# Optimization experiments

Hardware: AMD Instinct MI355X
Metric: run time of the kernel (lower is better)

Reference implementation:

```python
import jax, jax.numpy as jnp
import numpy as np
from jax import lax

IMG_H, IMG_W = 800, 800           # self.image_size
GRID = 64                         # feature map H=W
STRIDE = IMG_H // GRID            # torchvision AnchorGenerator stride
ANCHOR_SIZE = 32.0                # sizes=(32,), aspect_ratios=(1.0,)
PRE_NMS_TOP_N = 500
POST_NMS_TOP_N = 500
NMS_THRESH = 0.7
MIN_BOX_SIZE = 0.001
MIN_BOX_SCORE = 0.0


def make_anchors(h, w, stride):
    # torchvision single-size, ratio-1 base anchor centered at origin: [-16,-16,16,16]
    half = ANCHOR_SIZE / 2.0
    base = jnp.array([-half, -half, half, half], dtype=jnp.float32)
    sx = jnp.arange(w, dtype=jnp.float32) * stride
    sy = jnp.arange(h, dtype=jnp.float32) * stride
    yy, xx = jnp.meshgrid(sy, sx, indexing='ij')
    shifts = jnp.stack([xx, yy, xx, yy], axis=-1).reshape(-1, 4)  # [HW,4], row-major over (y,x)
    return shifts + base  # [HW,4] in (x1,y1,x2,y2)


def decode_boxes(reg, anchors):
    # reg: [B,N,4] (dx,dy,dw,dh); anchors: [N,4]
    wa = anchors[:, 2] - anchors[:, 0]
    ha = anchors[:, 3] - anchors[:, 1]
    cxa = anchors[:, 0] + 0.5 * wa
    cya = anchors[:, 1] + 0.5 * ha
    dx, dy, dw, dh = reg[..., 0], reg[..., 1], reg[..., 2], reg[..., 3]
    cx = dx * wa + cxa
    cy = dy * ha + cya
    w = jnp.exp(dw) * wa
    h = jnp.exp(dh) * ha
    return jnp.stack([cx - 0.5 * w, cy - 0.5 * h, cx + 0.5 * w, cy + 0.5 * h], axis=-1)


def clip_boxes(boxes):
    x = jnp.clip(boxes[..., 0::2], 0.0, float(IMG_W))
    y = jnp.clip(boxes[..., 1::2], 0.0, float(IMG_H))
    out = jnp.stack([x[..., 0], y[..., 0], x[..., 1], y[..., 1]], axis=-1)
    return out


def pairwise_iou(boxes):
    # boxes: [N,4] -> iou [N,N]
    area = (boxes[:, 2] - boxes[:, 0]) * (boxes[:, 3] - boxes[:, 1])
    lt = jnp.maximum(boxes[:, None, :2], boxes[None, :, :2])
    rb = jnp.minimum(boxes[:, None, 2:], boxes[None, :, 2:])
    wh = jnp.clip(rb - lt, 0.0)
    inter = wh[..., 0] * wh[..., 1]
    return inter / (area[:, None] + area[None, :] - inter + 1e-9)


def nms_keep(boxes, valid):
    # boxes already sorted by descending score (topk output). Greedy NMS.
    n = boxes.shape[0]
    iou = pairwise_iou(boxes)
    idx = jnp.arange(n)

    def body(i, keep):
        suppress = keep[i] & (iou[i] > NMS_THRESH) & (idx > i)
        return keep & jnp.logical_not(suppress)

    return lax.fori_loop(0, n, body, valid)


def setup_inputs() -> dict:
    key = jax.random.key(0)
    ks = jax.random.split(key, 4)
    B, C, H, W = 4, 512, GRID, GRID
    feature_map = jax.random.normal(ks[0], (B, C, H, W), dtype=jnp.float32)
    conv_w = jax.random.normal(ks[1], (512, 512, 3, 3), dtype=jnp.float32) * 0.02
    conv_b = jnp.zeros((512,), dtype=jnp.float32)
    score_w = jax.random.normal(ks[2], (1, 512), dtype=jnp.float32) * 0.01
    score_b = jnp.zeros((1,), dtype=jnp.float32)
    bbox_w = jax.random.normal(ks[3], (4, 512), dtype=jnp.float32) * 0.01
    bbox_b = jnp.zeros((4,), dtype=jnp.float32)
    return {"feature_map": feature_map, "conv_w": conv_w, "conv_b": conv_b,
            "score_w": score_w, "score_b": score_b, "bbox_w": bbox_w, "bbox_b": bbox_b}


def reference(feature_map, conv_w, conv_b, score_w, score_b, bbox_w, bbox_b):
    B, C, H, W = feature_map.shape
    # common_feature_extractor: 3x3 conv + ReLU
    f = lax.conv_general_dilated(feature_map, conv_w, (1, 1), 'SAME',
                                 dimension_numbers=('NCHW', 'OIHW', 'NCHW'))
    f = jax.nn.relu(f + conv_b[None, :, None, None])
    # 1x1 heads
    object_score = jnp.einsum('bchw,oc->bohw', f, score_w) + score_b[None, :, None, None]  # [B,1,H,W]
    bbox_reg = jnp.einsum('bchw,oc->bohw', f, bbox_w) + bbox_b[None, :, None, None]        # [B,4,H,W]
    # reshape (B,4,-1).permute(0,2,1) -> [B,N,4]
    reg = jnp.transpose(bbox_reg.reshape(B, 4, -1), (0, 2, 1))
    anchors = make_anchors(H, W, STRIDE)                 # [N,4]
    proposals = decode_boxes(reg, anchors)               # [B,N,4]
    logits = object_score.reshape(B, -1)                 # [B,N]
    # filter_proposals: topk on detached logits
    top_vals, top_idx = lax.top_k(lax.stop_gradient(logits), PRE_NMS_TOP_N)  # sorted desc
    props = jnp.take_along_axis(proposals, top_idx[..., None], axis=1)       # [B,500,4]
    probs = jax.nn.sigmoid(top_vals)                                          # [B,500]
    props = clip_boxes(props)
    ws = props[..., 2] - props[..., 0]
    hs = props[..., 3] - props[..., 1]
    valid = (ws >= MIN_BOX_SIZE) & (hs >= MIN_BOX_SIZE) & (probs >= MIN_BOX_SCORE)
    keep = jax.vmap(nms_keep)(props, valid)               # [B,500] (post_nms_top_n == pre, no truncation)
    final_props = props * keep[..., None].astype(props.dtype)
    final_scores = probs * keep.astype(probs.dtype)
    return f, final_props, final_scores, keep
```

## Files before the change

### kernel.cpp

```cpp
#include <hip/hip_runtime.h>
#include <math.h>

#define BB   4
#define CC   512
#define HH   64
#define WW   64
#define NN   4096
#define TOPK 500

typedef _Float16 half8 __attribute__((ext_vector_type(8)));
typedef float f32x16   __attribute__((ext_vector_type(16)));

__device__ __forceinline__ void split_f16(float v, _Float16& h, _Float16& l) {
    h = (_Float16)v;
    l = (_Float16)(v - (float)h);
}

__global__ __launch_bounds__(256) void prepack_w_kernel(
    const float* __restrict__ w, _Float16* __restrict__ wh,
    _Float16* __restrict__ wl)
{
    const int t = blockIdx.x * 256 + threadIdx.x;
    if (t >= 512 * 32) return;
    const int co = t & 511;
    const int cb = t >> 9;
    const float* src = w + (size_t)co * 4608 + cb * 144;
#pragma unroll
    for (int tap = 0; tap < 9; ++tap) {
        half8 h0, h1, l0, l1;
#pragma unroll
        for (int i = 0; i < 8; ++i) {
            _Float16 h, l;
            split_f16(src[i * 9 + tap] * 4096.0f, h, l);
            h0[i] = h; l0[i] = l;
            split_f16(src[(i + 8) * 9 + tap] * 4096.0f, h, l);
            h1[i] = h; l1[i] = l;
        }
        const size_t dst = ((size_t)(tap * 32 + cb) * 512 + co) * 16;
        *(half8*)(wh + dst)     = h0;
        *(half8*)(wh + dst + 8) = h1;
        *(half8*)(wl + dst)     = l0;
        *(half8*)(wl + dst + 8) = l1;
    }
}

__global__ __launch_bounds__(256) void conv3x3_mfma_kernel(
    const float* __restrict__ x, const _Float16* __restrict__ wh,
    const _Float16* __restrict__ wl, const float* __restrict__ bias,
    float* __restrict__ out)
{
    __shared__ __align__(16) _Float16 xs_h[4][66][24];
    __shared__ __align__(16) _Float16 xs_l[4][66][24];

    const int tid  = threadIdx.x;
    const int lane = tid & 63;
    const int wave = tid >> 6;
    const int wco  = wave & 1;
    const int wpx  = wave >> 1;
    const int kg   = lane >> 5;
    const int ln   = lane & 31;

    const int co_blk = blockIdx.x * 128;
    const int r0     = blockIdx.y * 2;
    const int b      = blockIdx.z;

    const float* xb = x + (size_t)b * CC * NN;

    const int s_ci   = tid & 15;
    const int s_sub  = tid >> 4;
    const int s_row  = s_sub & 3;
    const int s_colg = s_sub >> 2;

    f32x16 acc[2][2];
#pragma unroll
    for (int mt = 0; mt < 2; ++mt)
#pragma unroll
        for (int nt = 0; nt < 2; ++nt)
#pragma unroll
            for (int r = 0; r < 16; ++r) acc[mt][nt][r] = 0.f;

    half8 Ah[2][2], Al[2][2];

    for (int cb = 0; cb < 32; ++cb) {
        const int gr = r0 - 1 + s_row;
        float vals[16];
        if ((unsigned)gr < 64u) {
            const float* p = xb + (size_t)(cb * 16 + s_ci) * NN + gr * 64 + s_colg * 16;
            *(float4*)&vals[0]  = *(const float4*)(p + 0);
            *(float4*)&vals[4]  = *(const float4*)(p + 4);
            *(float4*)&vals[8]  = *(const float4*)(p + 8);
            *(float4*)&vals[12] = *(const float4*)(p + 12);
        } else {
#pragma unroll
            for (int j = 0; j < 16; ++j) vals[j] = 0.f;
        }
        __syncthreads();
#pragma unroll
        for (int j = 0; j < 16; ++j) {
            _Float16 h, l;
            split_f16(vals[j] * 4096.0f, h, l);
            const int c = 1 + s_colg * 16 + j;
            xs_h[s_row][c][s_ci] = h;
            xs_l[s_row][c][s_ci] = l;
        }
        if (tid < 128) {
            const int ci = tid & 15, rr = (tid >> 4) & 3, side = (tid >> 6) & 1;
            xs_h[rr][side * 65][ci] = (_Float16)0.f;
            xs_l[rr][side * 65][ci] = (_Float16)0.f;
        }
        __syncthreads();

        {
            const size_t base = (size_t)(0 * 32 + cb) * 512;
#pragma unroll
            for (int mt = 0; mt < 2; ++mt) {
                const int co_w = co_blk + wco * 64 + mt * 32 + ln;
                const size_t o = (base + co_w) * 16 + kg * 8;
                Ah[0][mt] = *(const half8*)(wh + o);
                Al[0][mt] = *(const half8*)(wl + o);
            }
        }
#pragma unroll
        for (int tap = 0; tap < 9; ++tap) {
            const int pb = tap & 1, pn = pb ^ 1;
            if (tap < 8) {
                const size_t base = (size_t)((tap + 1) * 32 + cb) * 512;
#pragma unroll
                for (int mt = 0; mt < 2; ++mt) {
                    const int co_w = co_blk + wco * 64 + mt * 32 + ln;
                    const size_t o = (base + co_w) * 16 + kg * 8;
                    Ah[pn][mt] = *(const half8*)(wh + o);
                    Al[pn][mt] = *(const half8*)(wl + o);
                }
            }
            const int dy = tap / 3, dx = tap % 3;
            half8 Bh[2], Bl[2];
#pragma unroll
            for (int nt = 0; nt < 2; ++nt) {
                const int c = nt * 32 + ln + dx;
                Bh[nt] = *(const half8*)&xs_h[wpx + dy][c][kg * 8];
                Bl[nt] = *(const half8*)&xs_l[wpx + dy][c][kg * 8];
            }
#pragma unroll
            for (int mt = 0; mt < 2; ++mt)
#pragma unroll
                for (int nt = 0; nt < 2; ++nt) {
                    acc[mt][nt] = __builtin_amdgcn_mfma_f32_32x32x16_f16(
                        Al[pb][mt], Bh[nt], acc[mt][nt], 0, 0, 0);
                    acc[mt][nt] = __builtin_amdgcn_mfma_f32_32x32x16_f16(
                        Ah[pb][mt], Bl[nt], acc[mt][nt], 0, 0, 0);
                    acc[mt][nt] = __builtin_amdgcn_mfma_f32_32x32x16_f16(
                        Ah[pb][mt], Bh[nt], acc[mt][nt], 0, 0, 0);
                }
        }
    }

    const float inv_scale = 5.9604644775390625e-08f;
    const int himg = r0 + wpx;
#pragma unroll
    for (int mt = 0; mt < 2; ++mt)
#pragma unroll
        for (int nt = 0; nt < 2; ++nt) {
            const int wimg = nt * 32 + ln;
#pragma unroll
            for (int reg = 0; reg < 16; ++reg) {
                const int co = co_blk + wco * 64 + mt * 32 +
                               (reg & 3) + 8 * (reg >> 2) + 4 * kg;
                float v = fmaf(acc[mt][nt][reg], inv_scale, bias[co]);
                v = v > 0.f ? v : 0.f;
                out[(((size_t)b * CC + co) * HH + himg) * WW + wimg] = v;
            }
        }
}

__global__ __launch_bounds__(256) void conv3x3_relu_kernel(
    const float* __restrict__ x, const float* __restrict__ wgt,
    const float* __restrict__ bias, float* __restrict__ out)
{
    __shared__ float xs[8][6][66];
    __shared__ float wsh[8][9][64];
    const int co_base = blockIdx.x * 64;
    const int r0 = blockIdx.y * 4;
    const int b  = blockIdx.z;
    const int tid = threadIdx.x;
    const int col = tid & 63;
    const int co_off = (tid >> 6) * 16;

    float acc[4][16];
#pragma unroll
    for (int r = 0; r < 4; ++r)
#pragma unroll
        for (int k = 0; k < 16; ++k) acc[r][k] = 0.f;

    const float* xb = x + (size_t)b * CC * HH * WW;

    for (int cb = 0; cb < CC; cb += 8) {
        __syncthreads();
        for (int idx = tid; idx < 8 * 6 * 66; idx += 256) {
            int cc = idx % 66;
            int rest = idx / 66;
            int rr = rest % 6;
            int ci = rest / 6;
            int gr = r0 - 1 + rr;
            int gc = cc - 1;
            float v = 0.f;
            if (gr >= 0 && gr < HH && (unsigned)gc < (unsigned)WW)
                v = xb[((cb + ci) * HH + gr) * WW + gc];
            xs[ci][rr][cc] = v;
        }
        for (int idx = tid; idx < 8 * 9 * 64; idx += 256) {
            int co = idx & 63;
            int rest = idx >> 6;
            int ci = rest / 9;
            int tap = rest - ci * 9;
            wsh[ci][tap][co] = wgt[(size_t)(co_base + co) * (CC * 9) + (cb + ci) * 9 + tap];
        }
        __syncthreads();
#pragma unroll
        for (int ci = 0; ci < 8; ++ci) {
#pragma unroll
            for (int kh = 0; kh < 3; ++kh) {
                float xv[4][3];
#pragma unroll
                for (int r = 0; r < 4; ++r)
#pragma unroll
                    for (int kw = 0; kw < 3; ++kw)
                        xv[r][kw] = xs[ci][r + kh][col + kw];
#pragma unroll
                for (int kw = 0; kw < 3; ++kw) {
#pragma unroll
                    for (int k = 0; k < 16; k += 4) {
                        float4 wv = *(const float4*)&wsh[ci][kh * 3 + kw][co_off + k];
#pragma unroll
                        for (int r = 0; r < 4; ++r) {
                            acc[r][k + 0] = fmaf(xv[r][kw], wv.x, acc[r][k + 0]);
                            acc[r][k + 1] = fmaf(xv[r][kw], wv.y, acc[r][k + 1]);
                            acc[r][k + 2] = fmaf(xv[r][kw], wv.z, acc[r][k + 2]);
                            acc[r][k + 3] = fmaf(xv[r][kw], wv.w, acc[r][k + 3]);
                        }
                    }
                }
            }
        }
    }
#pragma unroll
    for (int k = 0; k < 16; ++k) {
        const int co = co_base + co_off + k;
        const float bv = bias[co];
#pragma unroll
        for (int r = 0; r < 4; ++r) {
            float v = acc[r][k] + bv;
            v = v > 0.f ? v : 0.f;
            out[(((size_t)b * CC + co) * HH + (r0 + r)) * WW + col] = v;
        }
    }
}

__global__ __launch_bounds__(256) void heads_decode_kernel(
    const float* __restrict__ f, const float* __restrict__ score_w,
    const float* __restrict__ score_b, const float* __restrict__ bbox_w,
    const float* __restrict__ bbox_b,
    float* __restrict__ logits, float* __restrict__ props)
{
    __shared__ float sw[CC];
    __shared__ float bw0[CC], bw1[CC], bw2[CC], bw3[CC];
    const int tid = threadIdx.x;
    for (int i = tid; i < CC; i += 256) {
        sw[i]  = score_w[i];
        bw0[i] = bbox_w[0 * CC + i];
        bw1[i] = bbox_w[1 * CC + i];
        bw2[i] = bbox_w[2 * CC + i];
        bw3[i] = bbox_w[3 * CC + i];
    }
    __syncthreads();
    const int b = blockIdx.y;
    const int n = blockIdx.x * 256 + tid;
    const float* fb = f + (size_t)b * CC * NN + n;
    float s = 0.f, d0 = 0.f, d1 = 0.f, d2 = 0.f, d3 = 0.f;
    for (int ci = 0; ci < CC; ++ci) {
        float v = fb[(size_t)ci * NN];
        s  = fmaf(v, sw[ci],  s);
        d0 = fmaf(v, bw0[ci], d0);
        d1 = fmaf(v, bw1[ci], d1);
        d2 = fmaf(v, bw2[ci], d2);
        d3 = fmaf(v, bw3[ci], d3);
    }
    s  += score_b[0];
    d0 += bbox_b[0]; d1 += bbox_b[1]; d2 += bbox_b[2]; d3 += bbox_b[3];
    logits[b * NN + n] = s;
    const int hx = n & 63, hy = n >> 6;
    const float cxa = 12.f * (float)hx, cya = 12.f * (float)hy;
    const float cx = d0 * 32.f + cxa;
    const float cy = d1 * 32.f + cya;
    const float w2 = expf(d2) * 16.f;
    const float h2 = expf(d3) * 16.f;
    float* p = props + ((size_t)b * NN + n) * 4;
    p[0] = cx - w2; p[1] = cy - h2; p[2] = cx + w2; p[3] = cy + h2;
}

__global__ __launch_bounds__(1024) void topk_kernel(
    const float* __restrict__ logits, const float* __restrict__ props,
    float* __restrict__ props500, float* __restrict__ probs500,
    unsigned long long* __restrict__ validb)
{
    __shared__ float sv[NN];
    __shared__ int   si[NN];
    const int b = blockIdx.x;
    const int tid = threadIdx.x;
    for (int i = tid; i < NN; i += 1024) { sv[i] = logits[b * NN + i]; si[i] = i; }
    __syncthreads();
    for (int k = 2; k <= NN; k <<= 1) {
        for (int j = k >> 1; j > 0; j >>= 1) {
            for (int t = tid; t < NN / 2; t += 1024) {
                const int i = ((t & ~(j - 1)) << 1) | (t & (j - 1));
                const int l = i | j;
                const float av = sv[i], bv = sv[l];
                const int   ai = si[i], bi = si[l];
                const bool bef  = (av > bv) || (av == bv && ai < bi);
                const bool swap = ((i & k) == 0) ? !bef : bef;
                if (swap) { sv[i] = bv; si[i] = bi; sv[l] = av; si[l] = ai; }
            }
            __syncthreads();
        }
    }
    if (tid < 512) {
        bool val = false;
        if (tid < TOPK) {
            const int n  = si[tid];
            const float v = sv[tid];
            const float* p = props + ((size_t)b * NN + n) * 4;
            const float x1 = fminf(fmaxf(p[0], 0.f), 800.f);
            const float y1 = fminf(fmaxf(p[1], 0.f), 800.f);
            const float x2 = fminf(fmaxf(p[2], 0.f), 800.f);
            const float y2 = fminf(fmaxf(p[3], 0.f), 800.f);
            const float pr = 1.f / (1.f + expf(-v));
            float* q = props500 + ((size_t)b * TOPK + tid) * 4;
            q[0] = x1; q[1] = y1; q[2] = x2; q[3] = y2;
            probs500[b * TOPK + tid] = pr;
            val = ((x2 - x1) >= 0.001f) && ((y2 - y1) >= 0.001f) && (pr >= 0.f);
        }
        const unsigned long long m = __ballot(val);
        if ((tid & 63) == 0) validb[b * 8 + (tid >> 6)] = m;
    }
}

__global__ __launch_bounds__(256) void nms_mask_kernel(
    const float* __restrict__ props500, unsigned long long* __restrict__ mask)
{
    const int gid = blockIdx.x * 256 + threadIdx.x;
    if (gid >= BB * TOPK * 8) return;
    const int wword = gid & 7;
    const int rest = gid >> 3;
    const int i = rest % TOPK;
    const int b = rest / TOPK;
    const float* bp = props500 + (size_t)b * TOPK * 4;
    const float x1 = bp[i * 4 + 0], y1 = bp[i * 4 + 1];
    const float x2 = bp[i * 4 + 2], y2 = bp[i * 4 + 3];
    const float ai = (x2 - x1) * (y2 - y1);
    unsigned long long m = 0ull;
    for (int bit = 0; bit < 64; ++bit) {
        const int j = wword * 64 + bit;
        if (j >= TOPK) break;
        if (j <= i) continue;
        const float u1 = bp[j * 4 + 0], v1 = bp[j * 4 + 1];
        const float u2 = bp[j * 4 + 2], v2 = bp[j * 4 + 3];
        const float aj = (u2 - u1) * (v2 - v1);
        const float lx = fmaxf(x1, u1), ly = fmaxf(y1, v1);
        const float rx = fminf(x2, u2), ry = fminf(y2, v2);
        const float iw = fmaxf(rx - lx, 0.f), ih = fmaxf(ry - ly, 0.f);
        const float inter = iw * ih;
        const float iou = inter / (ai + aj - inter + 1e-9f);
        if (iou > 0.7f) m |= (1ull << bit);
    }
    mask[gid] = m;
}

__global__ __launch_bounds__(256) void nms_finalize_kernel(
    const unsigned long long* __restrict__ mask,
    const unsigned long long* __restrict__ validb,
    const float* __restrict__ props500, const float* __restrict__ probs500,
    float* __restrict__ out_props, float* __restrict__ out_scores,
    float* __restrict__ out_keep)
{
    __shared__ unsigned long long sm[TOPK * 8];
    __shared__ unsigned long long sk[8];
    const int b = blockIdx.x;
    const int tid = threadIdx.x;
    for (int i = tid; i < TOPK * 8; i += 256) sm[i] = mask[(size_t)b * TOPK * 8 + i];
    if (tid < 8) sk[tid] = validb[b * 8 + tid];
    __syncthreads();
    if (tid == 0) {
        unsigned long long kw[8];
#pragma unroll
        for (int w = 0; w < 8; ++w) kw[w] = sk[w];
#pragma unroll
        for (int wi = 0; wi < 8; ++wi) {
            const int lim = (wi == 7) ? (TOPK - 7 * 64) : 64;
            for (int bi = 0; bi < lim; ++bi) {
                const unsigned long long keepbit = (kw[wi] >> bi) & 1ull;
                const unsigned long long sel = 0ull - keepbit;
                const int i = wi * 64 + bi;
#pragma unroll
                for (int w = 0; w < 8; ++w) kw[w] &= ~(sm[i * 8 + w] & sel);
            }
        }
#pragma unroll
        for (int w = 0; w < 8; ++w) sk[w] = kw[w];
    }
    __syncthreads();
    for (int t = tid; t < TOPK; t += 256) {
        const float fk = (float)((sk[t >> 6] >> (t & 63)) & 1ull);
        const float* q = props500 + ((size_t)b * TOPK + t) * 4;
        float* o = out_props + ((size_t)b * TOPK + t) * 4;
        o[0] = q[0] * fk; o[1] = q[1] * fk; o[2] = q[2] * fk; o[3] = q[3] * fk;
        out_scores[b * TOPK + t] = probs500[b * TOPK + t] * fk;
        out_keep[b * TOPK + t]   = fk;
    }
}

extern "C" void kernel_launch(void* const* d_in, const int* in_sizes, int n_in,
                              void* d_out, int out_size, void* d_ws, size_t ws_size,
                              hipStream_t stream)
{
    const float* x       = (const float*)d_in[0];
    const float* conv_w  = (const float*)d_in[1];
    const float* conv_b  = (const float*)d_in[2];
    const float* score_w = (const float*)d_in[3];
    const float* score_b = (const float*)d_in[4];
    const float* bbox_w  = (const float*)d_in[5];
    const float* bbox_b  = (const float*)d_in[6];

    float* f_out      = (float*)d_out;
    float* out_props  = f_out + (size_t)BB * CC * HH * WW;
    float* out_scores = out_props + BB * TOPK * 4;
    float* out_keep   = out_scores + BB * TOPK;

    const size_t WPE = (size_t)9 * 32 * 512 * 16;
    const size_t WP_BYTES = WPE * 2 * sizeof(_Float16);
    const size_t SCRATCH_BYTES =
        (size_t)BB * NN * 4 + (size_t)BB * NN * 16 + (size_t)BB * TOPK * 16 +
        (size_t)BB * TOPK * 4 + (size_t)BB * 8 * 8 + (size_t)BB * TOPK * 8 * 8 + 256;
    const bool use_mfma = (ws_size >= WP_BYTES + SCRATCH_BYTES);

    _Float16* wph = (_Float16*)d_ws;
    _Float16* wpl = wph + WPE;
    char* scratch = use_mfma ? (char*)(wpl + WPE) : (char*)d_ws;

    float* logits   = (float*)scratch;
    float* props    = logits + BB * NN;
    float* props500 = props + BB * NN * 4;
    float* probs500 = props500 + BB * TOPK * 4;
    unsigned long long* validb = (unsigned long long*)(probs500 + BB * TOPK);
    unsigned long long* maskp  = validb + BB * 8;

    if (use_mfma) {
        prepack_w_kernel<<<64, 256, 0, stream>>>(conv_w, wph, wpl);
        conv3x3_mfma_kernel<<<dim3(4, 32, BB), 256, 0, stream>>>(x, wph, wpl, conv_b, f_out);
    } else {
        conv3x3_relu_kernel<<<dim3(8, 16, BB), 256, 0, stream>>>(x, conv_w, conv_b, f_out);
    }
    heads_decode_kernel<<<dim3(16, BB), 256, 0, stream>>>(f_out, score_w, score_b,
                                                          bbox_w, bbox_b, logits, props);
    topk_kernel<<<BB, 1024, 0, stream>>>(logits, props, props500, probs500, validb);
    nms_mask_kernel<<<(BB * TOPK * 8 + 255) / 256, 256, 0, stream>>>(props500, maskp);
    nms_finalize_kernel<<<BB, 256, 0, stream>>>(maskp, validb, props500, probs500,
                                                out_props, out_scores, out_keep);
}
```

Before: 500.4 us.

## Double-buffer conv input tiles, pack top-k sort keys, widen heads grid

The MFMA conv kernel now double-buffers the shared-memory input tile. It prefetches the next channel block's global loads during the tap loop and prefetches B fragments one tap ahead, so there is one barrier per channel block instead of two. It also sets a min-blocks-per-CU launch bound. The top-k bitonic sort packs score and index into a single 64-bit key, cutting shared-memory traffic and compare work. The heads kernel uses 64-thread blocks over 4x more blocks to spread the memory-bound reduction across more CUs. The doubled LDS use and the register bound may limit occupancy or cause spills.

```diff
diff --git a/kernel.cpp b/kernel.cpp
--- a/kernel.cpp
+++ b/kernel.cpp
@@ -44,13 +44,13 @@
     }
 }
 
-__global__ __launch_bounds__(256) void conv3x3_mfma_kernel(
+__global__ __launch_bounds__(256, 2) void conv3x3_mfma_kernel(
     const float* __restrict__ x, const _Float16* __restrict__ wh,
     const _Float16* __restrict__ wl, const float* __restrict__ bias,
     float* __restrict__ out)
 {
-    __shared__ __align__(16) _Float16 xs_h[4][66][24];
-    __shared__ __align__(16) _Float16 xs_l[4][66][24];
+    __shared__ __align__(16) _Float16 xs_h[2][4][66][24];
+    __shared__ __align__(16) _Float16 xs_l[2][4][66][24];
 
     const int tid  = threadIdx.x;
     const int lane = tid & 63;
@@ -70,6 +70,17 @@
     const int s_sub  = tid >> 4;
     const int s_row  = s_sub & 3;
     const int s_colg = s_sub >> 2;
+    const int gr     = r0 - 1 + s_row;
+    const bool gr_ok = ((unsigned)gr < 64u);
+    const float* xrow = xb + (size_t)s_ci * NN + gr * 64 + s_colg * 16;
+
+    if (tid < 128) {
+        const int ci = tid & 15, rr = (tid >> 4) & 3, side = (tid >> 6) & 1;
+        xs_h[0][rr][side * 65][ci] = (_Float16)0.f;
+        xs_l[0][rr][side * 65][ci] = (_Float16)0.f;
+        xs_h[1][rr][side * 65][ci] = (_Float16)0.f;
+        xs_l[1][rr][side * 65][ci] = (_Float16)0.f;
+    }
 
     f32x16 acc[2][2];
 #pragma unroll
@@ -80,78 +91,92 @@
             for (int r = 0; r < 16; ++r) acc[mt][nt][r] = 0.f;
 
     half8 Ah[2][2], Al[2][2];
+    half8 Bh[2][2], Bl[2][2];
+
+    const int co_w0  = co_blk + wco * 64 + ln;
+    const size_t aoff0 = (size_t)co_w0 * 16 + kg * 8;
+    const size_t aoff1 = aoff0 + 32 * 16;
+
+    float vals[16];
+#pragma unroll
+    for (int j = 0; j < 16; ++j) vals[j] = 0.f;
+
+    if (gr_ok) {
+        *(float4*)&vals[0]  = *(const float4*)(xrow + 0);
+        *(float4*)&vals[4]  = *(const float4*)(xrow + 4);
+        *(float4*)&vals[8]  = *(const float4*)(xrow + 8);
+        *(float4*)&vals[12] = *(const float4*)(xrow + 12);
+    }
+#pragma unroll
+    for (int j = 0; j < 16; ++j) {
+        _Float16 h, l;
+        split_f16(vals[j] * 4096.0f, h, l);
+        const int c = 1 + s_colg * 16 + j;
+        xs_h[0][s_row][c][s_ci] = h;
+        xs_l[0][s_row][c][s_ci] = l;
+    }
+    __syncthreads();
+    int buf = 0;
 
     for (int cb = 0; cb < 32; ++cb) {
-        const int gr = r0 - 1 + s_row;
-        float vals[16];
-        if ((unsigned)gr < 64u) {
-            const float* p = xb + (size_t)(cb * 16 + s_ci) * NN + gr * 64 + s_colg * 16;
-            *(float4*)&vals[0]  = *(const float4*)(p + 0);
-            *(float4*)&vals[4]  = *(const float4*)(p + 4);
-            *(float4*)&vals[8]  = *(const float4*)(p + 8);
-            *(float4*)&vals[12] = *(const float4*)(p + 12);
-        } else {
-#pragma unroll
-            for (int j = 0; j < 16; ++j) vals[j] = 0.f;
-        }
-        __syncthreads();
-#pragma unroll
-        for (int j = 0; j < 16; ++j) {
-            _Float16 h, l;
-            split_f16(vals[j] * 4096.0f, h, l);
-            const int c = 1 + s_colg * 16 + j;
-            xs_h[s_row][c][s_ci] = h;
-            xs_l[s_row][c][s_ci] = l;
-        }
-        if (tid < 128) {
-            const int ci = tid & 15, rr = (tid >> 4) & 3, side = (tid >> 6) & 1;
-            xs_h[rr][side * 65][ci] = (_Float16)0.f;
-            xs_l[rr][side * 65][ci] = (_Float16)0.f;
-        }
-        __syncthreads();
-
         {
-            const size_t base = (size_t)(0 * 32 + cb) * 512;
-#pragma unroll
-            for (int mt = 0; mt < 2; ++mt) {
-                const int co_w = co_blk + wco * 64 + mt * 32 + ln;
-                const size_t o = (base + co_w) * 16 + kg * 8;
-                Ah[0][mt] = *(const half8*)(wh + o);
-                Al[0][mt] = *(const half8*)(wl + o);
-            }
+            const size_t ab = (size_t)(0 * 32 + cb) * 8192;
+            Ah[0][0] = *(const half8*)(wh + ab + aoff0);
+            Al[0][0] = *(const half8*)(wl + ab + aoff0);
+            Ah[0][1] = *(const half8*)(wh + ab + aoff1);
+            Al[0][1] = *(const half8*)(wl + ab + aoff1);
+            Bh[0][0] = *(const half8*)&xs_h[buf][wpx][ln][kg * 8];
+            Bl[0][0] = *(const half8*)&xs_l[buf][wpx][ln][kg * 8];
+            Bh[0][1] = *(const half8*)&xs_h[buf][wpx][32 + ln][kg * 8];
+            Bl[0][1] = *(const half8*)&xs_l[buf][wpx][32 + ln][kg * 8];
         }
 #pragma unroll
         for (int tap = 0; tap < 9; ++tap) {
             const int pb = tap & 1, pn = pb ^ 1;
             if (tap < 8) {
-                const size_t base = (size_t)((tap + 1) * 32 + cb) * 512;
-#pragma unroll
-                for (int mt = 0; mt < 2; ++mt) {
-                    const int co_w = co_blk + wco * 64 + mt * 32 + ln;
-                    const size_t o = (base + co_w) * 16 + kg * 8;
-                    Ah[pn][mt] = *(const half8*)(wh + o);
-                    Al[pn][mt] = *(const half8*)(wl + o);
-                }
-            }
-            const int dy = tap / 3, dx = tap % 3;
-            half8 Bh[2], Bl[2];
-#pragma unroll
-            for (int nt = 0; nt < 2; ++nt) {
-                const int c = nt * 32 + ln + dx;
-                Bh[nt] = *(const half8*)&xs_h[wpx + dy][c][kg * 8];
-                Bl[nt] = *(const half8*)&xs_l[wpx + dy][c][kg * 8];
+                const int t1 = tap + 1;
+                const size_t ab = (size_t)(t1 * 32 + cb) * 8192;
+                Ah[pn][0] = *(const half8*)(wh + ab + aoff0);
+                Al[pn][0] = *(const half8*)(wl + ab + aoff0);
+                Ah[pn][1] = *(const half8*)(wh + ab + aoff1);
+                Al[pn][1] = *(const half8*)(wl + ab + aoff1);
+                const int dy1 = t1 / 3, dx1 = t1 % 3;
+                Bh[pn][0] = *(const half8*)&xs_h[buf][wpx + dy1][ln + dx1][kg * 8];
+                Bl[pn][0] = *(const half8*)&xs_l[buf][wpx + dy1][ln + dx1][kg * 8];
+                Bh[pn][1] = *(const half8*)&xs_h[buf][wpx + dy1][32 + ln + dx1][kg * 8];
+                Bl[pn][1] = *(const half8*)&xs_l[buf][wpx + dy1][32 + ln + dx1][kg * 8];
+            }
+            if (tap == 7 && cb < 31 && gr_ok) {
+                const float* p = xrow + (size_t)(cb + 1) * 16 * NN;
+                *(float4*)&vals[0]  = *(const float4*)(p + 0);
+                *(float4*)&vals[4]  = *(const float4*)(p + 4);
+                *(float4*)&vals[8]  = *(const float4*)(p + 8);
+                *(float4*)&vals[12] = *(const float4*)(p + 12);
             }
 #pragma unroll
             for (int mt = 0; mt < 2; ++mt)
 #pragma unroll
                 for (int nt = 0; nt < 2; ++nt) {
                     acc[mt][nt] = __builtin_amdgcn_mfma_f32_32x32x16_f16(
-                        Al[pb][mt], Bh[nt], acc[mt][nt], 0, 0, 0);
+                        Al[pb][mt], Bh[pb][nt], acc[mt][nt], 0, 0, 0);
                     acc[mt][nt] = __builtin_amdgcn_mfma_f32_32x32x16_f16(
-                        Ah[pb][mt], Bl[nt], acc[mt][nt], 0, 0, 0);
+                        Ah[pb][mt], Bl[pb][nt], acc[mt][nt], 0, 0, 0);
                     acc[mt][nt] = __builtin_amdgcn_mfma_f32_32x32x16_f16(
-                        Ah[pb][mt], Bh[nt], acc[mt][nt], 0, 0, 0);
+                        Ah[pb][mt], Bh[pb][nt], acc[mt][nt], 0, 0, 0);
                 }
+        }
+        if (cb < 31) {
+            const int nb = buf ^ 1;
+#pragma unroll
+            for (int j = 0; j < 16; ++j) {
+                _Float16 h, l;
+                split_f16(vals[j] * 4096.0f, h, l);
+                const int c = 1 + s_colg * 16 + j;
+                xs_h[nb][s_row][c][s_ci] = h;
+                xs_l[nb][s_row][c][s_ci] = l;
+            }
+            __syncthreads();
+            buf = nb;
         }
     }
 
@@ -256,7 +281,7 @@
     }
 }
 
-__global__ __launch_bounds__(256) void heads_decode_kernel(
+__global__ __launch_bounds__(64) void heads_decode_kernel(
     const float* __restrict__ f, const float* __restrict__ score_w,
     const float* __restrict__ score_b, const float* __restrict__ bbox_w,
     const float* __restrict__ bbox_b,
@@ -265,7 +290,7 @@
     __shared__ float sw[CC];
     __shared__ float bw0[CC], bw1[CC], bw2[CC], bw3[CC];
     const int tid = threadIdx.x;
-    for (int i = tid; i < CC; i += 256) {
+    for (int i = tid; i < CC; i += 64) {
         sw[i]  = score_w[i];
         bw0[i] = bbox_w[0 * CC + i];
         bw1[i] = bbox_w[1 * CC + i];
@@ -274,7 +299,7 @@
     }
     __syncthreads();
     const int b = blockIdx.y;
-    const int n = blockIdx.x * 256 + tid;
+    const int n = blockIdx.x * 64 + tid;
     const float* fb = f + (size_t)b * CC * NN + n;
     float s = 0.f, d0 = 0.f, d1 = 0.f, d2 = 0.f, d3 = 0.f;
     for (int ci = 0; ci < CC; ++ci) {
@@ -303,22 +328,24 @@
     float* __restrict__ props500, float* __restrict__ probs500,
     unsigned long long* __restrict__ validb)
 {
-    __shared__ float sv[NN];
-    __shared__ int   si[NN];
+    __shared__ unsigned long long skey[NN];
     const int b = blockIdx.x;
     const int tid = threadIdx.x;
-    for (int i = tid; i < NN; i += 1024) { sv[i] = logits[b * NN + i]; si[i] = i; }
+    for (int i = tid; i < NN; i += 1024) {
+        const unsigned u = __float_as_uint(logits[b * NN + i]);
+        const unsigned k32 = u ^ ((u >> 31) ? 0xFFFFFFFFu : 0x80000000u);
+        skey[i] = ((unsigned long long)k32 << 32) | (unsigned)(NN - 1 - i);
+    }
     __syncthreads();
     for (int k = 2; k <= NN; k <<= 1) {
         for (int j = k >> 1; j > 0; j >>= 1) {
             for (int t = tid; t < NN / 2; t += 1024) {
                 const int i = ((t & ~(j - 1)) << 1) | (t & (j - 1));
                 const int l = i | j;
-                const float av = sv[i], bv = sv[l];
-                const int   ai = si[i], bi = si[l];
-                const bool bef  = (av > bv) || (av == bv && ai < bi);
+                const unsigned long long a = skey[i], c = skey[l];
+                const bool bef  = (a > c);
                 const bool swap = ((i & k) == 0) ? !bef : bef;
-                if (swap) { sv[i] = bv; si[i] = bi; sv[l] = av; si[l] = ai; }
+                if (swap) { skey[i] = c; skey[l] = a; }
             }
             __syncthreads();
         }
@@ -326,8 +353,11 @@
     if (tid < 512) {
         bool val = false;
         if (tid < TOPK) {
-            const int n  = si[tid];
-            const float v = sv[tid];
+            const unsigned long long K = skey[tid];
+            const int n = NN - 1 - (int)(K & 0xFFFFFFFFu);
+            const unsigned k32 = (unsigned)(K >> 32);
+            const unsigned u = (k32 & 0x80000000u) ? (k32 ^ 0x80000000u) : ~k32;
+            const float v = __uint_as_float(u);
             const float* p = props + ((size_t)b * NN + n) * 4;
             const float x1 = fminf(fmaxf(p[0], 0.f), 800.f);
             const float y1 = fminf(fmaxf(p[1], 0.f), 800.f);
@@ -459,8 +489,8 @@
     } else {
         conv3x3_relu_kernel<<<dim3(8, 16, BB), 256, 0, stream>>>(x, conv_w, conv_b, f_out);
     }
-    heads_decode_kernel<<<dim3(16, BB), 256, 0, stream>>>(f_out, score_w, score_b,
-                                                          bbox_w, bbox_b, logits, props);
+    heads_decode_kernel<<<dim3(64, BB), 64, 0, stream>>>(f_out, score_w, score_b,
+                                                         bbox_w, bbox_b, logits, props);
     topk_kernel<<<BB, 1024, 0, stream>>>(logits, props, props500, probs500, validb);
     nms_mask_kernel<<<(BB * TOPK * 8 + 255) / 256, 256, 0, stream>>>(props500, maskp);
     nms_finalize_kernel<<<BB, 256, 0, stream>>>(maskp, validb, props500, probs500,
```

Measured after the change: 458.0 us. 1.09x faster.
